# Kernel tuning notes

Measured on AMD Instinct MI355X. Metric: run time of the kernel, lower is better.

The kernel has to match this reference:

```python
import jax, jax.numpy as jnp
import numpy as np

# Grid config: xbound [0,90,0.6], ybound [-15,15,0.15], zbound [-10,10,20]
DX = np.array([0.6, 0.15, 20.0], dtype=np.float32)                 # voxel sizes
BX = np.array([0.0 + 0.3, -15.0 + 0.075, -10.0 + 10.0], dtype=np.float32)  # voxel-center origins
NX = (150, 200, 1)                                                 # voxels per axis


def setup_inputs() -> dict:
    key = jax.random.key(0)
    k1, k2, k3, k4 = jax.random.split(key, 4)
    B, N, D, H, W, C = 4, 6, 59, 16, 44, 64
    shp = (B, N, D, H, W)
    # ego-frame frustum point coordinates; ranges slightly exceed grid bounds
    gx = jax.random.uniform(k1, shp, jnp.float32, minval=-2.0, maxval=95.0)
    gy = jax.random.uniform(k2, shp, jnp.float32, minval=-17.0, maxval=17.0)
    gz = jax.random.uniform(k3, shp, jnp.float32, minval=-3.0, maxval=3.0)
    geom_feats = jnp.stack([gx, gy, gz], axis=-1)                  # [B,N,D,H,W,3]
    x = jax.random.normal(k4, shp + (C,), jnp.float32)             # [B,N,D,H,W,C]
    return {"geom_feats": geom_feats, "x": x}


def reference(geom_feats, x):
    """LSS voxel_pooling. The torch sort + cumsum + diff (QuickCumsum) computes the
    per-voxel sum of features; here expressed as a masked segment_sum (same math)."""
    B, N, D, H, W, C = x.shape
    Nprime = B * N * D * H * W
    nx0, nx1, nx2 = NX

    xf = x.reshape(Nprime, C)
    dx = jnp.asarray(DX)
    bx = jnp.asarray(BX)
    # torch .long() truncates toward zero; astype(int32) matches that
    g = ((geom_feats - (bx - dx / 2.0)) / dx).astype(jnp.int32).reshape(Nprime, 3)

    batch_ix = jnp.repeat(jnp.arange(B, dtype=jnp.int32), Nprime // B)  # [Nprime]

    kept = ((g[:, 0] >= 0) & (g[:, 0] < nx0)
            & (g[:, 1] >= 0) & (g[:, 1] < nx1)
            & (g[:, 2] >= 0) & (g[:, 2] < nx2))

    ranks = (g[:, 0] * (nx1 * nx2 * B)
             + g[:, 1] * (nx2 * B)
             + g[:, 2] * B
             + batch_ix)
    total = nx0 * nx1 * nx2 * B
    seg = jnp.where(kept, ranks, total)  # dropped points -> dummy segment

    pooled = jax.ops.segment_sum(jnp.where(kept[:, None], xf, 0.0), seg,
                                 num_segments=total + 1)[:total]   # [nx0*nx1*nx2*B, C]

    final = pooled.reshape(nx0, nx1, nx2, B, C).transpose(3, 4, 2, 0, 1)  # [B,C,Z,X,Y]
    # torch.cat(final.unbind(dim=2), 1) -> [B, C*Z, X, Y]
    out = jnp.concatenate([final[:, :, z] for z in range(nx2)], axis=1)
    return out
```

## Files before the change

kernel.cpp:

```cpp
#include <hip/hip_runtime.h>


#define NPRIME 996864
#define NCH 64
#define NX0 150
#define NX1 200
#define CELLS_PER_B (NX0 * NX1)
#define NCELLS (4 * CELLS_PER_B)
#define BATCH_STRIDE (NPRIME / 4)
#define CAP 44
#define CNT_BYTES ((size_t)NCELLS * 4)
#define SLOT_BYTES ((size_t)NCELLS * CAP * 4)
#define CELL_BYTES ((size_t)NPRIME * 4)

__device__ __forceinline__ int bin_recip(float v, float off, float rcp) {
    float num = v - off;
    float q   = num * rcp;
    return (int)q;
}

__device__ __forceinline__ int compute_cell(float gx, float gy, float gz, int p) {
    int i0 = bin_recip(gx,   0.0f, 1.0f / 0.6f);
    int i1 = bin_recip(gy, -15.0f, 1.0f / 0.15f);
    int i2 = bin_recip(gz, -10.0f, 1.0f / 20.0f);
    bool kept = (i0 >= 0) & (i0 < NX0) & (i1 >= 0) & (i1 < NX1) & (i2 >= 0) & (i2 < 1);
    int b = p / BATCH_STRIDE;
    return kept ? (b * CELLS_PER_B + i0 * NX1 + i1) : -1;
}

__global__ __launch_bounds__(256) void lss_zero(unsigned* __restrict__ cnt) {
    int i = blockIdx.x * 256 + threadIdx.x;
    if (i < NCELLS) cnt[i] = 0u;
}

__global__ __launch_bounds__(256) void lss_bin_push(
    const float* __restrict__ geom,
    unsigned* __restrict__ cnt,
    int* __restrict__ slots)
{
    int p = blockIdx.x * 256 + threadIdx.x;
    if (p >= NPRIME) return;
    float gx = geom[3 * p + 0];
    float gy = geom[3 * p + 1];
    float gz = geom[3 * p + 2];
    int c = compute_cell(gx, gy, gz, p);
    if (c < 0) return;
    unsigned pos = atomicAdd(&cnt[c], 1u);
    if (pos < CAP) slots[c * CAP + pos] = p;
}

__global__ __launch_bounds__(1024) void lss_accum(
    const float* __restrict__ x,
    const unsigned* __restrict__ cnt,
    const int* __restrict__ slots,
    float* __restrict__ out)
{
    __shared__ float tile[64][65];
    int b    = blockIdx.y;
    int xy0  = blockIdx.x * 64;
    int t    = threadIdx.x;
    int wave = t >> 6;
    int lane = t & 63;

    #pragma unroll
    for (int j = 0; j < 4; ++j) {
        int xyl = wave * 4 + j;
        int xy  = xy0 + xyl;
        float a0 = 0.0f, a1 = 0.0f, a2 = 0.0f, a3 = 0.0f;
        if (xy < CELLS_PER_B) {
            int cell = b * CELLS_PER_B + xy;
            int n = (int)cnt[cell];
            if (n > CAP) n = CAP;
            const int* sl = slots + (size_t)cell * CAP;
            for (int i = 0; i < n; i += 4) {
                int i1 = i + 1 < n ? i + 1 : i;
                int i2 = i + 2 < n ? i + 2 : i;
                int i3 = i + 3 < n ? i + 3 : i;
                int p0 = sl[i],  p1 = sl[i1], p2 = sl[i2], p3 = sl[i3];
                float v0 = x[(size_t)p0 * NCH + lane];
                float v1 = x[(size_t)p1 * NCH + lane];
                float v2 = x[(size_t)p2 * NCH + lane];
                float v3 = x[(size_t)p3 * NCH + lane];
                a0 += v0;
                a1 += (i + 1 < n) ? v1 : 0.0f;
                a2 += (i + 2 < n) ? v2 : 0.0f;
                a3 += (i + 3 < n) ? v3 : 0.0f;
            }
        }
        tile[xyl][lane] = (a0 + a1) + (a2 + a3);
    }
    __syncthreads();

    int c   = t >> 4;
    int xyl = (t & 15) * 4;
    int xy  = xy0 + xyl;
    if (xy + 3 < CELLS_PER_B) {
        float4 w;
        w.x = tile[xyl + 0][c];
        w.y = tile[xyl + 1][c];
        w.z = tile[xyl + 2][c];
        w.w = tile[xyl + 3][c];
        *reinterpret_cast<float4*>(out + ((size_t)(b * NCH + c)) * CELLS_PER_B + xy) = w;
    }
}

__global__ __launch_bounds__(256) void lss_bin(
    const float* __restrict__ geom, int* __restrict__ cell)
{
    int p = blockIdx.x * 256 + threadIdx.x;
    if (p >= NPRIME) return;
    cell[p] = compute_cell(geom[3 * p], geom[3 * p + 1], geom[3 * p + 2], p);
}

__global__ __launch_bounds__(256) void lss_scatter_direct(
    const float* __restrict__ x, const int* __restrict__ cell,
    float* __restrict__ out)
{
    int t = blockIdx.x * 256 + threadIdx.x;
    int p = t >> 4;
    if (p >= NPRIME) return;
    int c = cell[p];
    if (c < 0) return;
    int c4 = (t & 15) << 2;
    const float4 xv = *reinterpret_cast<const float4*>(x + (size_t)p * NCH + c4);
    int b  = c / CELLS_PER_B;
    int xy = c - b * CELLS_PER_B;
    float* o = out + ((size_t)(b * NCH + c4)) * CELLS_PER_B + xy;
    atomicAdd(o,                   xv.x);
    atomicAdd(o +     CELLS_PER_B, xv.y);
    atomicAdd(o + 2 * CELLS_PER_B, xv.z);
    atomicAdd(o + 3 * CELLS_PER_B, xv.w);
}

__global__ __launch_bounds__(256) void lss_fused(
    const float* __restrict__ geom, const float* __restrict__ x,
    float* __restrict__ out)
{
    int t = blockIdx.x * 256 + threadIdx.x;
    int p = t >> 4;
    if (p >= NPRIME) return;
    int c = compute_cell(geom[3 * p], geom[3 * p + 1], geom[3 * p + 2], p);
    if (c < 0) return;
    int b  = c / CELLS_PER_B;
    int xy = c - b * CELLS_PER_B;
    int c4 = (t & 15) << 2;
    const float4 xv = *reinterpret_cast<const float4*>(x + (size_t)p * NCH + c4);
    float* o = out + ((size_t)(b * NCH + c4)) * CELLS_PER_B + xy;
    atomicAdd(o,                   xv.x);
    atomicAdd(o +     CELLS_PER_B, xv.y);
    atomicAdd(o + 2 * CELLS_PER_B, xv.z);
    atomicAdd(o + 3 * CELLS_PER_B, xv.w);
}

extern "C" void kernel_launch(void* const* d_in, const int* in_sizes, int n_in,
                              void* d_out, int out_size, void* d_ws, size_t ws_size,
                              hipStream_t stream) {
    const float* geom = (const float*)d_in[0];
    const float* x    = (const float*)d_in[1];
    float* out = (float*)d_out;

    const int bin_blocks = (NPRIME + 255) / 256;

    if (ws_size >= CNT_BYTES + SLOT_BYTES) {
        unsigned* cnt = (unsigned*)d_ws;
        int* slots    = (int*)((char*)d_ws + CNT_BYTES);
        lss_zero<<<(NCELLS + 255) / 256, 256, 0, stream>>>(cnt);
        lss_bin_push<<<bin_blocks, 256, 0, stream>>>(geom, cnt, slots);
        dim3 agrid((CELLS_PER_B + 63) / 64, 4);
        lss_accum<<<agrid, 1024, 0, stream>>>(x, cnt, slots, out);
    } else if (ws_size >= CELL_BYTES) {
        int* cell = (int*)d_ws;
        hipMemsetAsync(d_out, 0, (size_t)out_size * sizeof(float), stream);
        lss_bin<<<bin_blocks, 256, 0, stream>>>(geom, cell);
        lss_scatter_direct<<<(NPRIME * 16 + 255) / 256, 256, 0, stream>>>(x, cell, out);
    } else {
        hipMemsetAsync(d_out, 0, (size_t)out_size * sizeof(float), stream);
        lss_fused<<<(NPRIME * 16 + 255) / 256, 256, 0, stream>>>(geom, x, out);
    }
}
```

Before: 125.9 us.

## Gather four points per wave with float4 loads and butterfly-reduce in lss_accum

```diff
diff --git a/kernel.cpp b/kernel.cpp
--- a/kernel.cpp
+++ b/kernel.cpp
@@ -61,33 +61,56 @@
     int t    = threadIdx.x;
     int wave = t >> 6;
     int lane = t & 63;
-
+    int rowsel = lane >> 4;
+    int chq    = (lane & 15) * 4;
+
+    int xyW = xy0 + wave * 4;
+    int n_[4];
+    const int* sl_[4];
     #pragma unroll
-    for (int j = 0; j < 4; ++j) {
-        int xyl = wave * 4 + j;
-        int xy  = xy0 + xyl;
-        float a0 = 0.0f, a1 = 0.0f, a2 = 0.0f, a3 = 0.0f;
-        if (xy < CELLS_PER_B) {
-            int cell = b * CELLS_PER_B + xy;
-            int n = (int)cnt[cell];
-            if (n > CAP) n = CAP;
-            const int* sl = slots + (size_t)cell * CAP;
-            for (int i = 0; i < n; i += 4) {
-                int i1 = i + 1 < n ? i + 1 : i;
-                int i2 = i + 2 < n ? i + 2 : i;
-                int i3 = i + 3 < n ? i + 3 : i;
-                int p0 = sl[i],  p1 = sl[i1], p2 = sl[i2], p3 = sl[i3];
-                float v0 = x[(size_t)p0 * NCH + lane];
-                float v1 = x[(size_t)p1 * NCH + lane];
-                float v2 = x[(size_t)p2 * NCH + lane];
-                float v3 = x[(size_t)p3 * NCH + lane];
-                a0 += v0;
-                a1 += (i + 1 < n) ? v1 : 0.0f;
-                a2 += (i + 2 < n) ? v2 : 0.0f;
-                a3 += (i + 3 < n) ? v3 : 0.0f;
+    for (int q = 0; q < 4; ++q) {
+        int xy = xyW + q;
+        int cell = b * CELLS_PER_B + xy;
+        int n = (xy < CELLS_PER_B) ? (int)cnt[cell] : 0;
+        n_[q]  = n > CAP ? CAP : n;
+        sl_[q] = slots + (size_t)cell * CAP;
+    }
+
+    float4 acc0 = {0,0,0,0}, acc1 = {0,0,0,0}, acc2 = {0,0,0,0}, acc3 = {0,0,0,0};
+    int nmax = max(max(n_[0], n_[1]), max(n_[2], n_[3]));
+
+    for (int i = 0; i < nmax; i += 4) {
+        #define GATHER(Q, ACC)                                                    \
+            if (i < n_[Q]) {                                                      \
+                int jj = i + rowsel;                                              \
+                int j  = jj < n_[Q] ? jj : 0;                                     \
+                unsigned p = min((unsigned)sl_[Q][j], NPRIME - 1u);               \
+                const float4 v = *reinterpret_cast<const float4*>(                \
+                    x + (size_t)p * NCH + chq);                                   \
+                if (jj < n_[Q]) { ACC.x += v.x; ACC.y += v.y;                     \
+                                  ACC.z += v.z; ACC.w += v.w; }                   \
             }
-        }
-        tile[xyl][lane] = (a0 + a1) + (a2 + a3);
+        GATHER(0, acc0)
+        GATHER(1, acc1)
+        GATHER(2, acc2)
+        GATHER(3, acc3)
+        #undef GATHER
+    }
+
+    #define BFLY(ACC)                                                             \
+        ACC.x += __shfl_xor(ACC.x, 16); ACC.y += __shfl_xor(ACC.y, 16);           \
+        ACC.z += __shfl_xor(ACC.z, 16); ACC.w += __shfl_xor(ACC.w, 16);           \
+        ACC.x += __shfl_xor(ACC.x, 32); ACC.y += __shfl_xor(ACC.y, 32);           \
+        ACC.z += __shfl_xor(ACC.z, 32); ACC.w += __shfl_xor(ACC.w, 32);
+    BFLY(acc0) BFLY(acc1) BFLY(acc2) BFLY(acc3)
+    #undef BFLY
+
+    if (lane < 16) {
+        int c0 = lane * 4;
+        *reinterpret_cast<float4*>(&tile[wave * 4 + 0][c0]) = acc0;
+        *reinterpret_cast<float4*>(&tile[wave * 4 + 1][c0]) = acc1;
+        *reinterpret_cast<float4*>(&tile[wave * 4 + 2][c0]) = acc2;
+        *reinterpret_cast<float4*>(&tile[wave * 4 + 3][c0]) = acc3;
     }
     __syncthreads();
 
```

Measured after the change: 121.7 us. -3.4%, faster.
